# Kernel optimization log

Measured on AMD Instinct MI355X. Metric: run time of the kernel, lower is better.

The kernel has to match this reference:

```python
import jax, jax.numpy as jnp
import numpy as np

N_NODES = 200_000
N_EVENTS = 50_000
MEM = 128
RAW = 64
TD = 64
HEADS = 2
DH = MEM // HEADS
EDGE_DIM = RAW + TD
MSG_IN = 2 * MEM + RAW + TD


def _time_enc(x, w, b):
    # PyG TimeEncoder: cos(Linear(t)) with Linear(1, time_dim)
    return jnp.cos(x[..., None] * w + b)


def setup_inputs() -> dict:
    key = jax.random.key(0)
    ks = jax.random.split(key, 30)

    def w(i, shape, scale=None):
        s = scale if scale is not None else 1.0 / np.sqrt(shape[-1])
        return jax.random.normal(ks[i], shape, jnp.float32) * s

    src = jax.random.randint(ks[0], (N_EVENTS,), 0, N_NODES)
    dst = jax.random.randint(ks[1], (N_EVENTS,), 0, N_NODES)
    t = jnp.sort(jax.random.uniform(ks[2], (N_EVENTS,), jnp.float32, 0.0, 1e4))
    return dict(
        memory=w(3, (N_NODES, MEM), 1.0),
        last_update=jnp.zeros((N_NODES,), jnp.float32),
        t=t,
        msg=w(4, (N_EVENTS, RAW), 1.0),
        src=src, dst=dst,
        time_w=w(5, (TD,), 1.0), time_b=w(6, (TD,), 1.0),
        gru_Wih=w(7, (3 * MEM, MSG_IN)), gru_bih=w(8, (3 * MEM,), 0.02),
        gru_Whh=w(9, (3 * MEM, MEM)), gru_bhh=w(10, (3 * MEM,), 0.02),
        Wq=w(11, (MEM, MEM)), bq=w(12, (MEM,), 0.02),
        Wk=w(13, (MEM, MEM)), bk=w(14, (MEM,), 0.02),
        Wv=w(15, (MEM, MEM)), bv=w(16, (MEM,), 0.02),
        We=w(17, (MEM, EDGE_DIM)),
        Wskip=w(18, (MEM, MEM)), bskip=w(19, (MEM,), 0.02),
        Wls=w(20, (MEM, MEM)), bls=w(21, (MEM,), 0.02),
        Wld=w(22, (MEM, MEM)), bld=w(23, (MEM,), 0.02),
        Wlf=w(24, (1, MEM)), blf=w(25, (1,), 0.02),
    )


def reference(memory, last_update, t, msg, src, dst, time_w, time_b,
              gru_Wih, gru_bih, gru_Whh, gru_bhh,
              Wq, bq, Wk, bk, Wv, bv, We, Wskip, bskip,
              Wls, bls, Wld, bld, Wlf, blf):
    N, D = memory.shape
    E = src.shape[0]
    # --- 1. IdentityMessage: raw store for src side and dst side of each event ---
    dt_s = t - last_update[src]
    dt_d = t - last_update[dst]
    m_s = jnp.concatenate([memory[src], memory[dst], msg, _time_enc(dt_s, time_w, time_b)], -1)
    m_d = jnp.concatenate([memory[dst], memory[src], msg, _time_enc(dt_d, time_w, time_b)], -1)
    all_msg = jnp.concatenate([m_s, m_d], 0)        # [2E, MSG_IN]
    all_id = jnp.concatenate([src, dst], 0)         # [2E]
    all_t = jnp.concatenate([t, t], 0)              # [2E]
    # --- 2. LastAggregator: keep the latest message per target node ---
    pos = jnp.arange(2 * E, dtype=jnp.int32)
    last_pos = jnp.full((N,), -1, jnp.int32).at[all_id].max(pos)
    is_last = last_pos[all_id] == pos               # [2E], exactly one True per touched node
    # --- 3. GRUCell memory update (computed per message, scattered for the last one) ---
    h = memory[all_id]
    gi = all_msg @ gru_Wih.T + gru_bih
    gh = h @ gru_Whh.T + gru_bhh
    ir, iz, i_n = jnp.split(gi, 3, -1)
    hr, hz, h_n = jnp.split(gh, 3, -1)
    r = jax.nn.sigmoid(ir + hr)
    zg = jax.nn.sigmoid(iz + hz)
    n = jnp.tanh(i_n + r * h_n)
    h_new = (1.0 - zg) * n + zg * h
    memory_new = memory.at[all_id].add(jnp.where(is_last[:, None], h_new - h, 0.0))
    last_update_new = last_update.at[all_id].max(jnp.where(is_last, all_t, -jnp.inf))
    # --- 4. GraphAttentionEmbedding: TransformerConv(heads=2, edge_dim) in eval mode ---
    rel_t = last_update_new[src] - t
    edge_attr = jnp.concatenate([_time_enc(rel_t, time_w, time_b), msg], -1)  # [E, EDGE_DIM]
    e_proj = edge_attr @ We.T                                                  # [E, MEM]
    q = (memory_new @ Wq.T + bq).reshape(N, HEADS, DH)
    k = (memory_new[src] @ Wk.T + bk + e_proj).reshape(E, HEADS, DH)
    v = (memory_new[src] @ Wv.T + bv + e_proj).reshape(E, HEADS, DH)
    logit = jnp.einsum('ehd,ehd->eh', q[dst], k) / np.sqrt(DH).astype(np.float32)
    mx = jnp.full((N, HEADS), -jnp.inf, memory.dtype).at[dst].max(logit)
    a = jnp.exp(logit - mx[dst])
    denom = jax.ops.segment_sum(a, dst, num_segments=N)
    attn = a / denom[dst]                                                      # segment softmax over incoming edges
    out = jnp.zeros((N, HEADS, DH), memory.dtype).at[dst].add(attn[..., None] * v)
    z = out.reshape(N, D) + memory_new @ Wskip.T + bskip                       # root/skip connection
    # --- 5. LinkPredictor on event endpoints ---
    hlp = jax.nn.relu(z[src] @ Wls.T + bls + z[dst] @ Wld.T + bld)
    return hlp @ Wlf.T + blf                                                   # [E, 1]
```

## Files before the change

### kernel.cpp

```cpp
#include <hip/hip_runtime.h>
#include <math.h>

#define NN 200000
#define NE 50000
#define D 128
#define ZROW 256

#define WGRU_SZ  196608
#define WATTN_SZ 147456
#define WLNK2_SZ 65536

#define CVT0 102528
#define MEMB_V4 6400000
#define MSGB_V4 800000

__device__ __forceinline__ float frcp_(float x) { return __builtin_amdgcn_rcpf(x); }
__device__ __forceinline__ float fsig_(float x) { return frcp_(1.f + __expf(-x)); }
__device__ __forceinline__ float ftanh_(float x) {
    float xc = fminf(fmaxf(x, -15.f), 15.f);
    float t = __expf(2.f * xc);
    return (t - 1.f) * frcp_(t + 1.f);
}

__device__ __forceinline__ unsigned short f2bf(float f) {
    unsigned int u = __float_as_uint(f);
    u = (u + 0x7fffu + ((u >> 16) & 1u)) >> 16;
    return (unsigned short)u;
}
__device__ __forceinline__ float bf2f(unsigned short b) {
    return __uint_as_float(((unsigned int)b) << 16);
}

typedef short bf16x8 __attribute__((ext_vector_type(8)));
typedef float f32x4  __attribute__((ext_vector_type(4)));

__global__ void k_initprep(const float* __restrict__ Wih, const float* __restrict__ Whh,
                           const float* __restrict__ Wk, const float* __restrict__ Wv,
                           const float* __restrict__ Wq, const float* __restrict__ We,
                           const float* __restrict__ Wskip, const float* __restrict__ bskip,
                           const float* __restrict__ Wls, const float* __restrict__ Wld,
                           const float* __restrict__ bls, const float* __restrict__ bld,
                           const int* __restrict__ src, const int* __restrict__ dst,
                           const float* __restrict__ memory, const float* __restrict__ msg,
                           unsigned short* __restrict__ wgru,
                           unsigned short* __restrict__ wattn,
                           unsigned short* __restrict__ wlink2,
                           float* __restrict__ blink,
                           unsigned short* __restrict__ memb,
                           unsigned short* __restrict__ msgb,
                           int* __restrict__ last_pos, int* __restrict__ count) {
    int idx = blockIdx.x * 256 + threadIdx.x;
    if (idx == 0) *count = 0;
    if (idx < 2 * NE) {
        int id = (idx < NE) ? src[idx] : dst[idx - NE];
        atomicMax(&last_pos[id], idx + 1);
    }
    if (idx >= CVT0) {
        int j = idx - CVT0;
        if (j < MEMB_V4) {
            float4 v = ((const float4*)memory)[j];
            ushort4 b;
            b.x = f2bf(v.x); b.y = f2bf(v.y); b.z = f2bf(v.z); b.w = f2bf(v.w);
            ((ushort4*)memb)[j] = b;
        } else {
            j -= MEMB_V4;
            if (j < MSGB_V4) {
                float4 v = ((const float4*)msg)[j];
                ushort4 b;
                b.x = f2bf(v.x); b.y = f2bf(v.y); b.z = f2bf(v.z); b.w = f2bf(v.w);
                ((ushort4*)msgb)[j] = b;
            }
        }
        return;
    }
    float4 v;
    unsigned short* dstp;
    int ncopies, stride;
    if (idx < 49152) {
        int n = idx / 96;
        int c = (idx - n * 96) * 4;
        if (n < 384) {
            v = *(const float4*)&Wih[n * 384 + c];
            if (n < 256 && c < 128) {
                const float4 w2 = *(const float4*)&Whh[n * 128 + c];
                v.x += w2.x; v.y += w2.y; v.z += w2.z; v.w += w2.w;
            }
        } else {
            if (c >= 128) return;
            v = *(const float4*)&Whh[(n - 128) * 128 + c];
        }
        dstp = &wgru[n * 384 + c]; ncopies = 8; stride = WGRU_SZ;
    } else if (idx < 49152 + 36864) {
        int i2 = idx - 49152;
        int n = i2 / 96;
        int c = (i2 - n * 96) * 4;
        if (n < 256) {
            const float* Wm = (n < 128) ? Wk : Wv;
            int nn = n & 127;
            if (c < 128)       v = *(const float4*)&Wm[nn * 128 + c];
            else if (c < 256)  v = *(const float4*)&We[nn * 128 + (c - 128)];
            else return;
        } else {
            if (c < 256) return;
            v = *(const float4*)&Wq[(n - 256) * 128 + (c - 256)];
        }
        dstp = &wattn[n * 384 + c]; ncopies = 4; stride = WATTN_SZ;
    } else if (idx < 86016 + 8192) {
        int i4 = idx - 86016;
        int n = i4 >> 6;
        int c = (i4 & 63) * 4;
        int dc;
        if (c < 128) { v = *(const float4*)&Wls[n * 128 + c];        dc = c; }
        else         { v = *(const float4*)&Wld[n * 128 + (c - 128)]; dc = c + 128; }
        dstp = &wlink2[n * 512 + dc]; ncopies = 4; stride = WLNK2_SZ;
    } else if (idx < 94208 + 8192) {
        int i5 = idx - 94208;
        int n = i5 >> 6;
        int g = i5 & 63;
        const float* Wrow = (g < 32) ? &Wls[n * 128] : &Wld[n * 128];
        int c = (g & 31) * 4;
        float ax = 0.f, ay = 0.f, az = 0.f, aw = 0.f;
        for (int j = 0; j < 128; ++j) {
            float a = Wrow[j];
            const float4 ws = *(const float4*)&Wskip[j * 128 + c];
            ax += a * ws.x; ay += a * ws.y; az += a * ws.z; aw += a * ws.w;
        }
        ushort4 b4;
        b4.x = f2bf(ax); b4.y = f2bf(ay); b4.z = f2bf(az); b4.w = f2bf(aw);
        unsigned short* dp = &wlink2[n * 512 + ((g < 32) ? 128 : 384) + c];
        for (int r = 0; r < 4; ++r)
            *(ushort4*)(dp + (size_t)r * WLNK2_SZ) = b4;
        return;
    } else {
        int n = idx - 102400;
        float s = bls[n] + bld[n];
        for (int j = 0; j < 128; ++j)
            s += (Wls[n * 128 + j] + Wld[n * 128 + j]) * bskip[j];
        blink[n] = s;
        return;
    }
    ushort4 b;
    b.x = f2bf(v.x); b.y = f2bf(v.y); b.z = f2bf(v.z); b.w = f2bf(v.w);
    for (int r = 0; r < ncopies; ++r)
        *(ushort4*)(dstp + (size_t)r * stride) = b;
}

__global__ void k_compact(const int* __restrict__ src, const int* __restrict__ dst,
                          const int* __restrict__ last_pos,
                          const float* __restrict__ tp, const float* __restrict__ lup,
                          int* __restrict__ count, int* __restrict__ node2slot,
                          int* __restrict__ head,
                          int4* __restrict__ slot_aux,
                          float* __restrict__ lu_new) {
    int i = blockIdx.x * blockDim.x + threadIdx.x;
    if (i >= 2 * NE) return;
    int e  = (i < NE) ? i : i - NE;
    int id = (i < NE) ? src[e] : dst[e];
    if (last_pos[id] != i + 1) return;
    int s = atomicAdd(count, 1);
    node2slot[id] = s;
    head[s] = -1;
    int oth = (i < NE) ? dst[e] : src[e];
    float tt = tp[e];
    float lu = lup[id];
    lu_new[id] = fmaxf(lu, tt);
    int4 aux; aux.x = e; aux.y = oth; aux.z = __float_as_int(tt - lu); aux.w = id;
    slot_aux[s] = aux;
}

#define GMB 64
__global__ __launch_bounds__(512) void k_gru(
    const unsigned short* __restrict__ msgb,
    const float* __restrict__ twp, const float* __restrict__ tbp,
    const int4* __restrict__ slot_aux,
    const unsigned short* __restrict__ memb,
    const unsigned short* __restrict__ wgru_all,
    const float* __restrict__ bih, const float* __restrict__ bhh,
    const int* __restrict__ countp,
    unsigned short* __restrict__ zcat)
{
    __shared__ alignas(16) unsigned short Xs[64][392];
    int cnt = *countp;
    int base = blockIdx.x * GMB;
    if (base >= cnt) return;
    int tid = threadIdx.x;
    const unsigned short* __restrict__ wgru = wgru_all + (size_t)(blockIdx.x & 7) * WGRU_SZ;

    {
        int m = tid >> 3, li = tid & 7;
        int ii = base + m; if (ii >= cnt) ii = cnt - 1;
        const int4 aux = slot_aux[ii];
        int e = aux.x, oth = aux.y, id = aux.w;
        float dt = __int_as_float(aux.z);
        const uint4* idr  = (const uint4*)(memb + (size_t)id  * D);
        const uint4* othr = (const uint4*)(memb + (size_t)oth * D);
        uint4 A0 = idr[li],  A1 = idr[li + 8];
        uint4 B0 = othr[li], B1 = othr[li + 8];
        uint4 M0 = *(const uint4*)&msgb[e * 64 + li * 8];
        int c0 = li * 8;
        float cv[8];
        #pragma unroll
        for (int k = 0; k < 8; ++k)
            cv[k] = cosf(dt * twp[c0 + k] + tbp[c0 + k]);
        *(uint4*)&Xs[m][li * 8]        = A0;
        *(uint4*)&Xs[m][64 + li * 8]   = A1;
        *(uint4*)&Xs[m][128 + li * 8]  = B0;
        *(uint4*)&Xs[m][192 + li * 8]  = B1;
        *(uint4*)&Xs[m][256 + li * 8]  = M0;
        ushort4 t0, t1;
        t0.x = f2bf(cv[0]); t0.y = f2bf(cv[1]); t0.z = f2bf(cv[2]); t0.w = f2bf(cv[3]);
        t1.x = f2bf(cv[4]); t1.y = f2bf(cv[5]); t1.z = f2bf(cv[6]); t1.w = f2bf(cv[7]);
        *(ushort4*)&Xs[m][320 + c0]     = t0;
        *(ushort4*)&Xs[m][320 + c0 + 4] = t1;
    }
    __syncthreads();

    int lane = tid & 63, w = tid >> 6;
    int q = lane >> 4, l15 = lane & 15;
    int q8 = q * 8, w16 = w * 16;

    f32x4 acc[4][4];
    #pragma unroll
    for (int mt = 0; mt < 4; ++mt)
        #pragma unroll
        for (int g = 0; g < 4; ++g)
            acc[mt][g] = (f32x4)(0.0f);

#define GRU_STEP(NG)                                                                      \
    {                                                                                     \
        bf16x8 a[4];                                                                      \
        _Pragma("unroll")                                                                 \
        for (int mt = 0; mt < 4; ++mt) a[mt] = *(const bf16x8*)&Xs[mt * 16 + l15][k0 + q8]; \
        _Pragma("unroll")                                                                 \
        for (int g = 0; g < NG; ++g) {                                                    \
            const bf16x8 b = *(const bf16x8*)&wgru[(g * 128 + w16 + l15) * 384 + k0 + q8]; \
            _Pragma("unroll")                                                             \
            for (int mt = 0; mt < 4; ++mt)                                                \
                acc[mt][g] = __builtin_amdgcn_mfma_f32_16x16x32_bf16(a[mt], b, acc[mt][g], 0, 0, 0); \
        }                                                                                 \
    }

    #pragma unroll 2
    for (int ks = 0; ks < 4; ++ks) { int k0 = ks * 32; GRU_STEP(4) }
    #pragma unroll 2
    for (int ks = 4; ks < 12; ++ks) { int k0 = ks * 32; GRU_STEP(3) }
#undef GRU_STEP

    float nval[4][4];
    {
        int c = w16 + l15;
        float br  = bih[c]       + bhh[c];
        float bz  = bih[128 + c] + bhh[128 + c];
        float bin = bih[256 + c];
        float bhn = bhh[256 + c];
        #pragma unroll
        for (int mt = 0; mt < 4; ++mt) {
            #pragma unroll
            for (int reg = 0; reg < 4; ++reg) {
                int m = mt * 16 + q * 4 + reg;
                float r  = fsig_(acc[mt][0][reg] + br);
                float zg = fsig_(acc[mt][1][reg] + bz);
                float n  = ftanh_(acc[mt][2][reg] + bin + r * (acc[mt][3][reg] + bhn));
                float hv = bf2f(Xs[m][c]);
                nval[mt][reg] = (1.f - zg) * n + zg * hv;
            }
        }
    }

    __syncthreads();
    {
        int c = w16 + l15;
        #pragma unroll
        for (int mt = 0; mt < 4; ++mt)
            #pragma unroll
            for (int reg = 0; reg < 4; ++reg)
                Xs[mt * 16 + q * 4 + reg][c] = f2bf(nval[mt][reg]);
    }
    __syncthreads();

    {
        #pragma unroll
        for (int j = 0; j < 2; ++j) {
            int ch = tid + 512 * j;
            int m = ch >> 4, c8 = ch & 15;
            *(uint4*)&zcat[(size_t)(base + m) * ZROW + 128 + c8 * 8] =
                *(const uint4*)&Xs[m][c8 * 8];
        }
    }
}

#define AMB 32
__global__ __launch_bounds__(256) void k_attnA(
    const int* __restrict__ srcp, const int* __restrict__ dstp,
    const float* __restrict__ tp, const unsigned short* __restrict__ msgb,
    const float* __restrict__ twp, const float* __restrict__ tbp,
    const float* __restrict__ lu_new, const int* __restrict__ node2slot,
    const unsigned short* __restrict__ zcat,
    const unsigned short* __restrict__ wattn_all,
    const float* __restrict__ bq, const float* __restrict__ bk, const float* __restrict__ bv,
    unsigned short* __restrict__ vbuf, float* __restrict__ abuf,
    int* __restrict__ head, int* __restrict__ next)
{
    __shared__ alignas(16) unsigned short Xs[32][392];
    unsigned short (*kLb)[136] = (unsigned short(*)[136])(&Xs[0][0]);
    unsigned short (*qLb)[136] = (unsigned short(*)[136])(&Xs[0][0] + 4352);
    __shared__ float sa[AMB][2];
    __shared__ int sslot[AMB], sdslot[AMB];
    __shared__ float srel[AMB];
    int tid = threadIdx.x;
    int e0 = blockIdx.x * AMB;
    const unsigned short* __restrict__ wattn = wattn_all + (size_t)(blockIdx.x & 3) * WATTN_SZ;
    {
        int gid = blockIdx.x * 256 + tid;
        if (gid < NE) {
            int sl = node2slot[dstp[gid]];
            next[gid] = atomicExch(&head[sl], gid);
        }
    }
    if (tid < AMB) {
        int e = e0 + tid; if (e >= NE) e = NE - 1;
        int s = srcp[e], dd = dstp[e];
        sslot[tid]  = node2slot[s];
        sdslot[tid] = node2slot[dd];
        srel[tid] = lu_new[s] - tp[e];
    }
    __syncthreads();
    {
        int m = tid >> 3, li = tid & 7;
        int e = e0 + m; if (e >= NE) e = NE - 1;
        int ssl = sslot[m], dsl = sdslot[m];
        float rel = srel[m];
        uint4* xrow = (uint4*)&Xs[m][0];
        const uint4* srow = (const uint4*)&zcat[(size_t)ssl * ZROW + 128];
        const uint4* drow = (const uint4*)&zcat[(size_t)dsl * ZROW + 128];
        #pragma unroll
        for (int j = 0; j < 2; ++j) {
            xrow[li + 8 * j]      = srow[li + 8 * j];
            xrow[32 + li + 8 * j] = drow[li + 8 * j];
        }
        {
            int c0 = li * 8;
            ushort4 lo, hi;
            lo.x = f2bf(cosf(rel * twp[c0 + 0] + tbp[c0 + 0]));
            lo.y = f2bf(cosf(rel * twp[c0 + 1] + tbp[c0 + 1]));
            lo.z = f2bf(cosf(rel * twp[c0 + 2] + tbp[c0 + 2]));
            lo.w = f2bf(cosf(rel * twp[c0 + 3] + tbp[c0 + 3]));
            hi.x = f2bf(cosf(rel * twp[c0 + 4] + tbp[c0 + 4]));
            hi.y = f2bf(cosf(rel * twp[c0 + 5] + tbp[c0 + 5]));
            hi.z = f2bf(cosf(rel * twp[c0 + 6] + tbp[c0 + 6]));
            hi.w = f2bf(cosf(rel * twp[c0 + 7] + tbp[c0 + 7]));
            *(ushort4*)&Xs[m][128 + c0]     = lo;
            *(ushort4*)&Xs[m][128 + c0 + 4] = hi;
        }
        *(uint4*)&Xs[m][192 + li * 8] = *(const uint4*)&msgb[e * 64 + li * 8];
    }
    __syncthreads();

    int lane = tid & 63, w = tid >> 6;
    int q = lane >> 4, l15 = lane & 15;
    int q8 = q * 8;

    f32x4 acc[2][6];
    #pragma unroll
    for (int mt = 0; mt < 2; ++mt)
        #pragma unroll
        for (int jj = 0; jj < 6; ++jj) acc[mt][jj] = (f32x4)(0.0f);

    #pragma unroll 2
    for (int ks = 0; ks < 8; ++ks) {
        int k0 = ks * 32;
        const bf16x8 a0 = *(const bf16x8*)&Xs[l15][k0 + q8];
        const bf16x8 a1 = *(const bf16x8*)&Xs[16 + l15][k0 + q8];
        #pragma unroll
        for (int jj = 0; jj < 4; ++jj) {
            int nt = w + 4 * jj;
            const bf16x8 b = *(const bf16x8*)&wattn[(nt * 16 + l15) * 384 + k0 + q8];
            acc[0][jj] = __builtin_amdgcn_mfma_f32_16x16x32_bf16(a0, b, acc[0][jj], 0, 0, 0);
            acc[1][jj] = __builtin_amdgcn_mfma_f32_16x16x32_bf16(a1, b, acc[1][jj], 0, 0, 0);
        }
    }
    #pragma unroll 2
    for (int ks = 8; ks < 12; ++ks) {
        int k0 = ks * 32;
        const bf16x8 a0 = *(const bf16x8*)&Xs[l15][k0 + q8];
        const bf16x8 a1 = *(const bf16x8*)&Xs[16 + l15][k0 + q8];
        #pragma unroll
        for (int jj = 4; jj < 6; ++jj) {
            int nt = w + 4 * jj;
            const bf16x8 b = *(const bf16x8*)&wattn[(nt * 16 + l15) * 384 + k0 + q8];
            acc[0][jj] = __builtin_amdgcn_mfma_f32_16x16x32_bf16(a0, b, acc[0][jj], 0, 0, 0);
            acc[1][jj] = __builtin_amdgcn_mfma_f32_16x16x32_bf16(a1, b, acc[1][jj], 0, 0, 0);
        }
    }

    __syncthreads();

    float vreg[2][2][4];
    #pragma unroll
    for (int jj = 0; jj < 6; ++jj) {
        int nt = w + 4 * jj;
        int gate = nt >> 3;
        int ch = (nt & 7) * 16 + l15;
        float bias = (gate == 0) ? bk[ch] : (gate == 1) ? bv[ch] : bq[ch];
        #pragma unroll
        for (int mt = 0; mt < 2; ++mt)
            #pragma unroll
            for (int reg = 0; reg < 4; ++reg) {
                int m = mt * 16 + q * 4 + reg;
                float val = acc[mt][jj][reg] + bias;
                if (gate == 0)      kLb[m][ch] = f2bf(val);
                else if (gate == 2) qLb[m][ch] = f2bf(val);
                else                vreg[jj - 2][mt][reg] = val;
            }
    }
    __syncthreads();
    #pragma unroll
    for (int pr = 0; pr < 16; ++pr) {
        int p2 = pr * 4 + w;
        int m = p2 >> 1, h = p2 & 1;
        float prod = bf2f(qLb[m][h * 64 + lane]) * bf2f(kLb[m][h * 64 + lane]);
        #pragma unroll
        for (int off = 32; off; off >>= 1) prod += __shfl_down(prod, off);
        if (lane == 0) {
            float a = __expf(prod * 0.125f);
            sa[m][h] = a;
            if (e0 + m < NE) abuf[(e0 + m) * 2 + h] = a;
        }
    }
    __syncthreads();
    {
        unsigned short (*vL)[136] = qLb;
        #pragma unroll
        for (int jv = 0; jv < 2; ++jv) {
            int ch = w * 16 + jv * 64 + l15;
            int h = jv;
            #pragma unroll
            for (int mt = 0; mt < 2; ++mt)
                #pragma unroll
                for (int reg = 0; reg < 4; ++reg) {
                    int m = mt * 16 + q * 4 + reg;
                    vL[m][ch] = f2bf(sa[m][h] * vreg[jv][mt][reg]);
                }
        }
        __syncthreads();
        #pragma unroll
        for (int j = 0; j < 2; ++j) {
            int chunk = tid + 256 * j;
            int row = chunk >> 4, c8 = chunk & 15;
            if (e0 + row < NE)
                *(uint4*)&vbuf[(size_t)(e0 + row) * D + c8 * 8] = *(const uint4*)&vL[row][c8 * 8];
        }
    }
}

__global__ __launch_bounds__(256) void k_gather(
    const int* __restrict__ countp, const int* __restrict__ head,
    const int* __restrict__ next, const float* __restrict__ abuf,
    const unsigned short* __restrict__ vbuf, unsigned short* __restrict__ zcat)
{
    int cnt = *countp;
    int slot = blockIdx.x * 32 + (threadIdx.x >> 3);
    if (slot >= cnt) return;
    int li = threadIdx.x & 7;
    int c0 = li * 16;
    int h = li >> 2;
    float vsum[16];
    #pragma unroll
    for (int j = 0; j < 16; ++j) vsum[j] = 0.f;
    float asum = 0.f;
    for (int e = head[slot]; e != -1; e = next[e]) {
        asum += abuf[e * 2 + h];
        uint4 v0 = *(const uint4*)&vbuf[(size_t)e * D + c0];
        uint4 v1 = *(const uint4*)&vbuf[(size_t)e * D + c0 + 8];
        const unsigned short* pv0 = (const unsigned short*)&v0;
        const unsigned short* pv1 = (const unsigned short*)&v1;
        #pragma unroll
        for (int j = 0; j < 8; ++j) { vsum[j] += bf2f(pv0[j]); vsum[8 + j] += bf2f(pv1[j]); }
    }
    float rr = (asum > 0.f) ? frcp_(asum) : 0.f;
    unsigned short o[16];
    #pragma unroll
    for (int j = 0; j < 16; ++j) o[j] = f2bf(vsum[j] * rr);
    *(uint4*)&zcat[(size_t)slot * ZROW + c0]     = *(const uint4*)&o[0];
    *(uint4*)&zcat[(size_t)slot * ZROW + c0 + 8] = *(const uint4*)&o[8];
}

#define ALB 32
__global__ __launch_bounds__(256) void k_link(
    const int* __restrict__ srcp, const int* __restrict__ dstp,
    const int* __restrict__ node2slot,
    const unsigned short* __restrict__ zcat,
    const unsigned short* __restrict__ wlink2_all,
    const float* __restrict__ blink,
    const float* __restrict__ Wlf, const float* __restrict__ blf,
    float* __restrict__ outp)
{
    __shared__ alignas(16) unsigned short Xs[32][520];
    __shared__ int ssl[32], sdl[32];
    __shared__ float sred[32][4];
    int tid = threadIdx.x;
    int e0 = blockIdx.x * ALB;
    const unsigned short* __restrict__ wlink2 = wlink2_all + (size_t)(blockIdx.x & 3) * WLNK2_SZ;
    if (tid < ALB) {
        int e = e0 + tid; if (e >= NE) e = NE - 1;
        ssl[tid] = node2slot[srcp[e]];
        sdl[tid] = node2slot[dstp[e]];
    }
    __syncthreads();
    {
        int m = tid >> 3, li = tid & 7;
        uint4* xrow = (uint4*)&Xs[m][0];
        const uint4* srow = (const uint4*)&zcat[(size_t)ssl[m] * ZROW];
        const uint4* drow = (const uint4*)&zcat[(size_t)sdl[m] * ZROW];
        #pragma unroll
        for (int j = 0; j < 4; ++j) {
            xrow[li + 8 * j]      = srow[li + 8 * j];
            xrow[32 + li + 8 * j] = drow[li + 8 * j];
        }
    }
    __syncthreads();

    int lane = tid & 63, w = tid >> 6;
    int q = lane >> 4, l15 = lane & 15;
    int q8 = q * 8;

    f32x4 acc[2][2];
    #pragma unroll
    for (int mt = 0; mt < 2; ++mt)
        #pragma unroll
        for (int jj = 0; jj < 2; ++jj) acc[mt][jj] = (f32x4)(0.0f);

    #pragma unroll 2
    for (int ks = 0; ks < 16; ++ks) {
        int k0 = ks * 32;
        bf16x8 a[2];
        #pragma unroll
        for (int mt = 0; mt < 2; ++mt) a[mt] = *(const bf16x8*)&Xs[mt * 16 + l15][k0 + q8];
        #pragma unroll
        for (int jj = 0; jj < 2; ++jj) {
            int nt = w + 4 * jj;
            const bf16x8 b = *(const bf16x8*)&wlink2[(nt * 16 + l15) * 512 + k0 + q8];
            #pragma unroll
            for (int mt = 0; mt < 2; ++mt)
                acc[mt][jj] = __builtin_amdgcn_mfma_f32_16x16x32_bf16(a[mt], b, acc[mt][jj], 0, 0, 0);
        }
    }

    float p[2][4];
    #pragma unroll
    for (int mt = 0; mt < 2; ++mt)
        #pragma unroll
        for (int reg = 0; reg < 4; ++reg) p[mt][reg] = 0.f;
    #pragma unroll
    for (int jj = 0; jj < 2; ++jj) {
        int ch = (w + 4 * jj) * 16 + l15;
        float bias = blink[ch];
        float wl = Wlf[ch];
        #pragma unroll
        for (int mt = 0; mt < 2; ++mt)
            #pragma unroll
            for (int reg = 0; reg < 4; ++reg)
                p[mt][reg] += fmaxf(acc[mt][jj][reg] + bias, 0.f) * wl;
    }
    #pragma unroll
    for (int mask = 1; mask < 16; mask <<= 1) {
        #pragma unroll
        for (int mt = 0; mt < 2; ++mt)
            #pragma unroll
            for (int reg = 0; reg < 4; ++reg)
                p[mt][reg] += __shfl_xor(p[mt][reg], mask);
    }
    if (l15 == 0) {
        #pragma unroll
        for (int mt = 0; mt < 2; ++mt)
            #pragma unroll
            for (int reg = 0; reg < 4; ++reg)
                sred[mt * 16 + q * 4 + reg][w] = p[mt][reg];
    }
    __syncthreads();
    if (tid < ALB) {
        int e = e0 + tid;
        if (e < NE)
            outp[e] = sred[tid][0] + sred[tid][1] + sred[tid][2] + sred[tid][3] + blf[0];
    }
}

extern "C" void kernel_launch(void* const* d_in, const int* in_sizes, int n_in,
                              void* d_out, int out_size, void* d_ws, size_t ws_size,
                              hipStream_t stream)
{
    const float* memory      = (const float*)d_in[0];
    const float* last_update = (const float*)d_in[1];
    const float* t           = (const float*)d_in[2];
    const float* msg         = (const float*)d_in[3];
    const int*   src         = (const int*)d_in[4];
    const int*   dst         = (const int*)d_in[5];
    const float* time_w      = (const float*)d_in[6];
    const float* time_b      = (const float*)d_in[7];
    const float* gru_Wih     = (const float*)d_in[8];
    const float* gru_bih     = (const float*)d_in[9];
    const float* gru_Whh     = (const float*)d_in[10];
    const float* gru_bhh     = (const float*)d_in[11];
    const float* Wq          = (const float*)d_in[12];
    const float* bq          = (const float*)d_in[13];
    const float* Wk          = (const float*)d_in[14];
    const float* bk          = (const float*)d_in[15];
    const float* Wv          = (const float*)d_in[16];
    const float* bv          = (const float*)d_in[17];
    const float* We          = (const float*)d_in[18];
    const float* Wskip       = (const float*)d_in[19];
    const float* bskip       = (const float*)d_in[20];
    const float* Wls         = (const float*)d_in[21];
    const float* bls         = (const float*)d_in[22];
    const float* Wld         = (const float*)d_in[23];
    const float* bld         = (const float*)d_in[24];
    const float* Wlf         = (const float*)d_in[25];
    const float* blf         = (const float*)d_in[26];
    float* outp = (float*)d_out;

    char* ws = (char*)d_ws;
    int*   last_pos  = (int*)  (ws + 0);
    int*   node2slot = (int*)  (ws + 800000);
    float* lu_new    = (float*)(ws + 1600000);
    int*   count     = (int*)  (ws + 2400000);
    unsigned short* wlink2  = (unsigned short*)(ws + 2800016);
    float* blink   = (float*)(ws + 3324304);
    int4*  slot_aux = (int4*)(ws + 4000000);
    unsigned short* memb    = (unsigned short*)(ws + 6000000);
    unsigned short* msgb    = (unsigned short*)(ws + 57200000);
    unsigned short* wgru    = (unsigned short*)(ws + 79624592);
    unsigned short* wattn   = (unsigned short*)(ws + 82770320);
    unsigned short* zcat    = (unsigned short*)(ws + 84474256);
    unsigned short* vbuf    = (unsigned short*)(ws + 135690640);
    float* abuf = (float*)(ws + 148490640);
    int*   head = (int*)  (ws + 148890640);
    int*   next = (int*)  (ws + 149290768);

    k_initprep<<<(CVT0 + MEMB_V4 + MSGB_V4 + 255) / 256, 256, 0, stream>>>(
                 gru_Wih, gru_Whh, Wk, Wv, Wq, We, Wskip, bskip, Wls, Wld, bls, bld,
                 src, dst, memory, msg, wgru, wattn, wlink2, blink, memb, msgb,
                 last_pos, count);
    k_compact <<<(2 * NE + 255) / 256, 256, 0, stream>>>(src, dst, last_pos,
                 t, last_update, count, node2slot, head, slot_aux, lu_new);
    k_gru     <<<(2 * NE + GMB - 1) / GMB, 512, 0, stream>>>(msgb, time_w, time_b,
                 slot_aux, memb, wgru, gru_bih, gru_bhh, count, zcat);
    k_attnA   <<<(NE + AMB - 1) / AMB, 256, 0, stream>>>(src, dst, t, msgb, time_w, time_b,
                 lu_new, node2slot, zcat, wattn, bq, bk, bv, vbuf, abuf, head, next);
    k_gather  <<<(2 * NE + 31) / 32, 256, 0, stream>>>(count, head, next, abuf, vbuf, zcat);
    k_link    <<<(NE + ALB - 1) / ALB, 256, 0, stream>>>(src, dst, node2slot, zcat,
                 wlink2, blink, Wlf, blf, outp);
}
```

Before: 426.2 us.

## Convert only touched memory rows to bf16 and shrink GRU tile to 32 rows

The full conversion of the 200k-row memory table to bf16 is replaced by a new kernel that converts only the rows of nodes touched by events into a compact per-slot buffer. It also remaps each slot's partner node to its slot index so the GRU can read the compact buffer directly. The GRU kernel changes from 64-row, 512-thread blocks to 32-row, 256-thread blocks, with each wave now covering two 16-column subtiles. This removes roughly 100 MB of memory traffic, at the cost of an extra launch and a random-row gather from fp32 memory.

```diff
diff --git a/kernel.cpp b/kernel.cpp
--- a/kernel.cpp
+++ b/kernel.cpp
@@ -11,7 +11,6 @@
 #define WLNK2_SZ 65536
 
 #define CVT0 102528
-#define MEMB_V4 6400000
 #define MSGB_V4 800000
 
 __device__ __forceinline__ float frcp_(float x) { return __builtin_amdgcn_rcpf(x); }
@@ -41,12 +40,11 @@
                            const float* __restrict__ Wls, const float* __restrict__ Wld,
                            const float* __restrict__ bls, const float* __restrict__ bld,
                            const int* __restrict__ src, const int* __restrict__ dst,
-                           const float* __restrict__ memory, const float* __restrict__ msg,
+                           const float* __restrict__ msg,
                            unsigned short* __restrict__ wgru,
                            unsigned short* __restrict__ wattn,
                            unsigned short* __restrict__ wlink2,
                            float* __restrict__ blink,
-                           unsigned short* __restrict__ memb,
                            unsigned short* __restrict__ msgb,
                            int* __restrict__ last_pos, int* __restrict__ count) {
     int idx = blockIdx.x * 256 + threadIdx.x;
@@ -57,19 +55,11 @@
     }
     if (idx >= CVT0) {
         int j = idx - CVT0;
-        if (j < MEMB_V4) {
-            float4 v = ((const float4*)memory)[j];
+        if (j < MSGB_V4) {
+            float4 v = ((const float4*)msg)[j];
             ushort4 b;
             b.x = f2bf(v.x); b.y = f2bf(v.y); b.z = f2bf(v.z); b.w = f2bf(v.w);
-            ((ushort4*)memb)[j] = b;
-        } else {
-            j -= MEMB_V4;
-            if (j < MSGB_V4) {
-                float4 v = ((const float4*)msg)[j];
-                ushort4 b;
-                b.x = f2bf(v.x); b.y = f2bf(v.y); b.z = f2bf(v.z); b.w = f2bf(v.w);
-                ((ushort4*)msgb)[j] = b;
-            }
+            ((ushort4*)msgb)[j] = b;
         }
         return;
     }
@@ -168,18 +158,40 @@
     slot_aux[s] = aux;
 }
 
-#define GMB 64
-__global__ __launch_bounds__(512) void k_gru(
+__global__ __launch_bounds__(256) void k_memcvt(
+    const float* __restrict__ memory, const int* __restrict__ node2slot,
+    const int* __restrict__ countp,
+    int4* __restrict__ slot_aux, unsigned short* __restrict__ mco)
+{
+    int cnt = *countp;
+    int s = blockIdx.x * 32 + (threadIdx.x >> 3);
+    if (s >= cnt) return;
+    int li = threadIdx.x & 7;
+    int4 aux = slot_aux[s];
+    const float4* mrow = (const float4*)(memory + (size_t)aux.w * D);
+    ushort4* orow = (ushort4*)(mco + (size_t)s * D);
+    #pragma unroll
+    for (int j = 0; j < 4; ++j) {
+        float4 v = mrow[li + 8 * j];
+        ushort4 b;
+        b.x = f2bf(v.x); b.y = f2bf(v.y); b.z = f2bf(v.z); b.w = f2bf(v.w);
+        orow[li + 8 * j] = b;
+    }
+    if (li == 0) slot_aux[s].y = node2slot[aux.y];
+}
+
+#define GMB 32
+__global__ __launch_bounds__(256) void k_gru(
     const unsigned short* __restrict__ msgb,
     const float* __restrict__ twp, const float* __restrict__ tbp,
     const int4* __restrict__ slot_aux,
-    const unsigned short* __restrict__ memb,
+    const unsigned short* __restrict__ mco,
     const unsigned short* __restrict__ wgru_all,
     const float* __restrict__ bih, const float* __restrict__ bhh,
     const int* __restrict__ countp,
     unsigned short* __restrict__ zcat)
 {
-    __shared__ alignas(16) unsigned short Xs[64][392];
+    __shared__ alignas(16) unsigned short Xs[32][392];
     int cnt = *countp;
     int base = blockIdx.x * GMB;
     if (base >= cnt) return;
@@ -190,10 +202,10 @@
         int m = tid >> 3, li = tid & 7;
         int ii = base + m; if (ii >= cnt) ii = cnt - 1;
         const int4 aux = slot_aux[ii];
-        int e = aux.x, oth = aux.y, id = aux.w;
+        int e = aux.x, oslot = aux.y;
         float dt = __int_as_float(aux.z);
-        const uint4* idr  = (const uint4*)(memb + (size_t)id  * D);
-        const uint4* othr = (const uint4*)(memb + (size_t)oth * D);
+        const uint4* idr  = (const uint4*)(mco + (size_t)ii    * D);
+        const uint4* othr = (const uint4*)(mco + (size_t)oslot * D);
         uint4 A0 = idr[li],  A1 = idr[li + 8];
         uint4 B0 = othr[li], B1 = othr[li + 8];
         uint4 M0 = *(const uint4*)&msgb[e * 64 + li * 8];
@@ -217,26 +229,31 @@
 
     int lane = tid & 63, w = tid >> 6;
     int q = lane >> 4, l15 = lane & 15;
-    int q8 = q * 8, w16 = w * 16;
-
-    f32x4 acc[4][4];
-    #pragma unroll
-    for (int mt = 0; mt < 4; ++mt)
+    int q8 = q * 8, w32 = w * 32;
+
+    f32x4 acc[2][4][2];
+    #pragma unroll
+    for (int mt = 0; mt < 2; ++mt)
         #pragma unroll
         for (int g = 0; g < 4; ++g)
-            acc[mt][g] = (f32x4)(0.0f);
+            #pragma unroll
+            for (int ns = 0; ns < 2; ++ns)
+                acc[mt][g][ns] = (f32x4)(0.0f);
 
 #define GRU_STEP(NG)                                                                      \
     {                                                                                     \
-        bf16x8 a[4];                                                                      \
+        bf16x8 a[2];                                                                      \
         _Pragma("unroll")                                                                 \
-        for (int mt = 0; mt < 4; ++mt) a[mt] = *(const bf16x8*)&Xs[mt * 16 + l15][k0 + q8]; \
+        for (int mt = 0; mt < 2; ++mt) a[mt] = *(const bf16x8*)&Xs[mt * 16 + l15][k0 + q8]; \
         _Pragma("unroll")                                                                 \
         for (int g = 0; g < NG; ++g) {                                                    \
-            const bf16x8 b = *(const bf16x8*)&wgru[(g * 128 + w16 + l15) * 384 + k0 + q8]; \
             _Pragma("unroll")                                                             \
-            for (int mt = 0; mt < 4; ++mt)                                                \
-                acc[mt][g] = __builtin_amdgcn_mfma_f32_16x16x32_bf16(a[mt], b, acc[mt][g], 0, 0, 0); \
+            for (int ns = 0; ns < 2; ++ns) {                                              \
+                const bf16x8 b = *(const bf16x8*)&wgru[(g * 128 + w32 + ns * 16 + l15) * 384 + k0 + q8]; \
+                _Pragma("unroll")                                                         \
+                for (int mt = 0; mt < 2; ++mt)                                            \
+                    acc[mt][g][ns] = __builtin_amdgcn_mfma_f32_16x16x32_bf16(a[mt], b, acc[mt][g][ns], 0, 0, 0); \
+            }                                                                             \
         }                                                                                 \
     }
 
@@ -246,42 +263,44 @@
     for (int ks = 4; ks < 12; ++ks) { int k0 = ks * 32; GRU_STEP(3) }
 #undef GRU_STEP
 
-    float nval[4][4];
-    {
-        int c = w16 + l15;
+    float nval[2][2][4];
+    #pragma unroll
+    for (int ns = 0; ns < 2; ++ns) {
+        int c = w32 + ns * 16 + l15;
         float br  = bih[c]       + bhh[c];
         float bz  = bih[128 + c] + bhh[128 + c];
         float bin = bih[256 + c];
         float bhn = bhh[256 + c];
         #pragma unroll
-        for (int mt = 0; mt < 4; ++mt) {
+        for (int mt = 0; mt < 2; ++mt) {
             #pragma unroll
             for (int reg = 0; reg < 4; ++reg) {
                 int m = mt * 16 + q * 4 + reg;
-                float r  = fsig_(acc[mt][0][reg] + br);
-                float zg = fsig_(acc[mt][1][reg] + bz);
-                float n  = ftanh_(acc[mt][2][reg] + bin + r * (acc[mt][3][reg] + bhn));
+                float r  = fsig_(acc[mt][0][ns][reg] + br);
+                float zg = fsig_(acc[mt][1][ns][reg] + bz);
+                float n  = ftanh_(acc[mt][2][ns][reg] + bin + r * (acc[mt][3][ns][reg] + bhn));
                 float hv = bf2f(Xs[m][c]);
-                nval[mt][reg] = (1.f - zg) * n + zg * hv;
+                nval[mt][ns][reg] = (1.f - zg) * n + zg * hv;
             }
         }
     }
 
     __syncthreads();
+    #pragma unroll
+    for (int ns = 0; ns < 2; ++ns) {
+        int c = w32 + ns * 16 + l15;
+        #pragma unroll
+        for (int mt = 0; mt < 2; ++mt)
+            #pragma unroll
+            for (int reg = 0; reg < 4; ++reg)
+                Xs[mt * 16 + q * 4 + reg][c] = f2bf(nval[mt][ns][reg]);
+    }
+    __syncthreads();
+
     {
-        int c = w16 + l15;
-        #pragma unroll
-        for (int mt = 0; mt < 4; ++mt)
-            #pragma unroll
-            for (int reg = 0; reg < 4; ++reg)
-                Xs[mt * 16 + q * 4 + reg][c] = f2bf(nval[mt][reg]);
-    }
-    __syncthreads();
-
-    {
         #pragma unroll
         for (int j = 0; j < 2; ++j) {
-            int ch = tid + 512 * j;
+            int ch = tid + 256 * j;
             int m = ch >> 4, c8 = ch & 15;
             *(uint4*)&zcat[(size_t)(base + m) * ZROW + 128 + c8 * 8] =
                 *(const uint4*)&Xs[m][c8 * 8];
@@ -626,7 +645,7 @@
     unsigned short* wlink2  = (unsigned short*)(ws + 2800016);
     float* blink   = (float*)(ws + 3324304);
     int4*  slot_aux = (int4*)(ws + 4000000);
-    unsigned short* memb    = (unsigned short*)(ws + 6000000);
+    unsigned short* mco     = (unsigned short*)(ws + 6000000);
     unsigned short* msgb    = (unsigned short*)(ws + 57200000);
     unsigned short* wgru    = (unsigned short*)(ws + 79624592);
     unsigned short* wattn   = (unsigned short*)(ws + 82770320);
@@ -636,14 +655,15 @@
     int*   head = (int*)  (ws + 148890640);
     int*   next = (int*)  (ws + 149290768);
 
-    k_initprep<<<(CVT0 + MEMB_V4 + MSGB_V4 + 255) / 256, 256, 0, stream>>>(
+    k_initprep<<<(CVT0 + MSGB_V4 + 255) / 256, 256, 0, stream>>>(
                  gru_Wih, gru_Whh, Wk, Wv, Wq, We, Wskip, bskip, Wls, Wld, bls, bld,
-                 src, dst, memory, msg, wgru, wattn, wlink2, blink, memb, msgb,
-                 last_pos, count);
+                 src, dst, msg, wgru, wattn, wlink2, blink, msgb, last_pos, count);
     k_compact <<<(2 * NE + 255) / 256, 256, 0, stream>>>(src, dst, last_pos,
                  t, last_update, count, node2slot, head, slot_aux, lu_new);
-    k_gru     <<<(2 * NE + GMB - 1) / GMB, 512, 0, stream>>>(msgb, time_w, time_b,
-                 slot_aux, memb, wgru, gru_bih, gru_bhh, count, zcat);
+    k_memcvt  <<<(2 * NE + 31) / 32, 256, 0, stream>>>(memory, node2slot, count,
+                 slot_aux, mco);
+    k_gru     <<<(2 * NE + GMB - 1) / GMB, 256, 0, stream>>>(msgb, time_w, time_b,
+                 slot_aux, mco, wgru, gru_bih, gru_bhh, count, zcat);
     k_attnA   <<<(NE + AMB - 1) / AMB, 256, 0, stream>>>(src, dst, t, msgb, time_w, time_b,
                  lu_new, node2slot, zcat, wattn, bq, bk, bv, vbuf, abuf, head, next);
     k_gather  <<<(2 * NE + 31) / 32, 256, 0, stream>>>(count, head, next, abuf, vbuf, zcat);
```

Result: slower. 465.9 us (+9.3%).

## Convert only touched memory rows to bf16 per slot; widen attention tile to 64 events

Applied to the files above, without the earlier changes.

Drops the full-table fp32-to-bf16 conversion of the node memory. A new kernel converts only the rows of nodes that appear in events, stores them compactly by slot, and rewrites each slot's partner id to its slot index so the GRU kernel reads compact rows. Separately, the attention kernel now processes 64 events per 512-thread block with a reorganised MFMA tiling, reusing each weight fragment across four row tiles. This removes large bandwidth-bound prep traffic at the cost of one extra launch and a serial dependency on compaction.

```diff
diff --git a/kernel.cpp b/kernel.cpp
--- a/kernel.cpp
+++ b/kernel.cpp
@@ -11,7 +11,6 @@
 #define WLNK2_SZ 65536
 
 #define CVT0 102528
-#define MEMB_V4 6400000
 #define MSGB_V4 800000
 
 __device__ __forceinline__ float frcp_(float x) { return __builtin_amdgcn_rcpf(x); }
@@ -41,12 +40,11 @@
                            const float* __restrict__ Wls, const float* __restrict__ Wld,
                            const float* __restrict__ bls, const float* __restrict__ bld,
                            const int* __restrict__ src, const int* __restrict__ dst,
-                           const float* __restrict__ memory, const float* __restrict__ msg,
+                           const float* __restrict__ msg,
                            unsigned short* __restrict__ wgru,
                            unsigned short* __restrict__ wattn,
                            unsigned short* __restrict__ wlink2,
                            float* __restrict__ blink,
-                           unsigned short* __restrict__ memb,
                            unsigned short* __restrict__ msgb,
                            int* __restrict__ last_pos, int* __restrict__ count) {
     int idx = blockIdx.x * 256 + threadIdx.x;
@@ -57,19 +55,11 @@
     }
     if (idx >= CVT0) {
         int j = idx - CVT0;
-        if (j < MEMB_V4) {
-            float4 v = ((const float4*)memory)[j];
+        if (j < MSGB_V4) {
+            float4 v = ((const float4*)msg)[j];
             ushort4 b;
             b.x = f2bf(v.x); b.y = f2bf(v.y); b.z = f2bf(v.z); b.w = f2bf(v.w);
-            ((ushort4*)memb)[j] = b;
-        } else {
-            j -= MEMB_V4;
-            if (j < MSGB_V4) {
-                float4 v = ((const float4*)msg)[j];
-                ushort4 b;
-                b.x = f2bf(v.x); b.y = f2bf(v.y); b.z = f2bf(v.z); b.w = f2bf(v.w);
-                ((ushort4*)msgb)[j] = b;
-            }
+            ((ushort4*)msgb)[j] = b;
         }
         return;
     }
@@ -168,12 +158,34 @@
     slot_aux[s] = aux;
 }
 
+__global__ __launch_bounds__(256) void k_memcvt(
+    const float* __restrict__ memory, const int* __restrict__ node2slot,
+    const int* __restrict__ countp,
+    int4* __restrict__ slot_aux, unsigned short* __restrict__ mco)
+{
+    int cnt = *countp;
+    int s = blockIdx.x * 32 + (threadIdx.x >> 3);
+    if (s >= cnt) return;
+    int li = threadIdx.x & 7;
+    int4 aux = slot_aux[s];
+    const float4* mrow = (const float4*)(memory + (size_t)aux.w * D);
+    ushort4* orow = (ushort4*)(mco + (size_t)s * D);
+    #pragma unroll
+    for (int j = 0; j < 4; ++j) {
+        float4 v = mrow[li + 8 * j];
+        ushort4 b;
+        b.x = f2bf(v.x); b.y = f2bf(v.y); b.z = f2bf(v.z); b.w = f2bf(v.w);
+        orow[li + 8 * j] = b;
+    }
+    if (li == 0) slot_aux[s].y = node2slot[aux.y];
+}
+
 #define GMB 64
 __global__ __launch_bounds__(512) void k_gru(
     const unsigned short* __restrict__ msgb,
     const float* __restrict__ twp, const float* __restrict__ tbp,
     const int4* __restrict__ slot_aux,
-    const unsigned short* __restrict__ memb,
+    const unsigned short* __restrict__ mco,
     const unsigned short* __restrict__ wgru_all,
     const float* __restrict__ bih, const float* __restrict__ bhh,
     const int* __restrict__ countp,
@@ -190,10 +202,10 @@
         int m = tid >> 3, li = tid & 7;
         int ii = base + m; if (ii >= cnt) ii = cnt - 1;
         const int4 aux = slot_aux[ii];
-        int e = aux.x, oth = aux.y, id = aux.w;
+        int e = aux.x, oslot = aux.y;
         float dt = __int_as_float(aux.z);
-        const uint4* idr  = (const uint4*)(memb + (size_t)id  * D);
-        const uint4* othr = (const uint4*)(memb + (size_t)oth * D);
+        const uint4* idr  = (const uint4*)(mco + (size_t)ii    * D);
+        const uint4* othr = (const uint4*)(mco + (size_t)oslot * D);
         uint4 A0 = idr[li],  A1 = idr[li + 8];
         uint4 B0 = othr[li], B1 = othr[li + 8];
         uint4 M0 = *(const uint4*)&msgb[e * 64 + li * 8];
@@ -289,8 +301,8 @@
     }
 }
 
-#define AMB 32
-__global__ __launch_bounds__(256) void k_attnA(
+#define AMB 64
+__global__ __launch_bounds__(512) void k_attnA(
     const int* __restrict__ srcp, const int* __restrict__ dstp,
     const float* __restrict__ tp, const unsigned short* __restrict__ msgb,
     const float* __restrict__ twp, const float* __restrict__ tbp,
@@ -301,9 +313,9 @@
     unsigned short* __restrict__ vbuf, float* __restrict__ abuf,
     int* __restrict__ head, int* __restrict__ next)
 {
-    __shared__ alignas(16) unsigned short Xs[32][392];
+    __shared__ alignas(16) unsigned short Xs[64][392];
     unsigned short (*kLb)[136] = (unsigned short(*)[136])(&Xs[0][0]);
-    unsigned short (*qLb)[136] = (unsigned short(*)[136])(&Xs[0][0] + 4352);
+    unsigned short (*qLb)[136] = (unsigned short(*)[136])(&Xs[0][0] + 8704);
     __shared__ float sa[AMB][2];
     __shared__ int sslot[AMB], sdslot[AMB];
     __shared__ float srel[AMB];
@@ -311,7 +323,7 @@
     int e0 = blockIdx.x * AMB;
     const unsigned short* __restrict__ wattn = wattn_all + (size_t)(blockIdx.x & 3) * WATTN_SZ;
     {
-        int gid = blockIdx.x * 256 + tid;
+        int gid = blockIdx.x * 512 + tid;
         if (gid < NE) {
             int sl = node2slot[dstp[gid]];
             next[gid] = atomicExch(&head[sl], gid);
@@ -360,63 +372,64 @@
     int q = lane >> 4, l15 = lane & 15;
     int q8 = q * 8;
 
-    f32x4 acc[2][6];
-    #pragma unroll
-    for (int mt = 0; mt < 2; ++mt)
-        #pragma unroll
-        for (int jj = 0; jj < 6; ++jj) acc[mt][jj] = (f32x4)(0.0f);
+    f32x4 acc[4][3];
+    #pragma unroll
+    for (int mt = 0; mt < 4; ++mt)
+        #pragma unroll
+        for (int jj = 0; jj < 3; ++jj) acc[mt][jj] = (f32x4)(0.0f);
 
     #pragma unroll 2
     for (int ks = 0; ks < 8; ++ks) {
         int k0 = ks * 32;
-        const bf16x8 a0 = *(const bf16x8*)&Xs[l15][k0 + q8];
-        const bf16x8 a1 = *(const bf16x8*)&Xs[16 + l15][k0 + q8];
-        #pragma unroll
-        for (int jj = 0; jj < 4; ++jj) {
-            int nt = w + 4 * jj;
+        bf16x8 a[4];
+        #pragma unroll
+        for (int mt = 0; mt < 4; ++mt) a[mt] = *(const bf16x8*)&Xs[mt * 16 + l15][k0 + q8];
+        #pragma unroll
+        for (int jj = 0; jj < 2; ++jj) {
+            int nt = w + 8 * jj;
             const bf16x8 b = *(const bf16x8*)&wattn[(nt * 16 + l15) * 384 + k0 + q8];
-            acc[0][jj] = __builtin_amdgcn_mfma_f32_16x16x32_bf16(a0, b, acc[0][jj], 0, 0, 0);
-            acc[1][jj] = __builtin_amdgcn_mfma_f32_16x16x32_bf16(a1, b, acc[1][jj], 0, 0, 0);
+            #pragma unroll
+            for (int mt = 0; mt < 4; ++mt)
+                acc[mt][jj] = __builtin_amdgcn_mfma_f32_16x16x32_bf16(a[mt], b, acc[mt][jj], 0, 0, 0);
         }
     }
     #pragma unroll 2
     for (int ks = 8; ks < 12; ++ks) {
         int k0 = ks * 32;
-        const bf16x8 a0 = *(const bf16x8*)&Xs[l15][k0 + q8];
-        const bf16x8 a1 = *(const bf16x8*)&Xs[16 + l15][k0 + q8];
-        #pragma unroll
-        for (int jj = 4; jj < 6; ++jj) {
-            int nt = w + 4 * jj;
-            const bf16x8 b = *(const bf16x8*)&wattn[(nt * 16 + l15) * 384 + k0 + q8];
-            acc[0][jj] = __builtin_amdgcn_mfma_f32_16x16x32_bf16(a0, b, acc[0][jj], 0, 0, 0);
-            acc[1][jj] = __builtin_amdgcn_mfma_f32_16x16x32_bf16(a1, b, acc[1][jj], 0, 0, 0);
-        }
-    }
-
-    __syncthreads();
-
-    float vreg[2][2][4];
-    #pragma unroll
-    for (int jj = 0; jj < 6; ++jj) {
-        int nt = w + 4 * jj;
-        int gate = nt >> 3;
-        int ch = (nt & 7) * 16 + l15;
-        float bias = (gate == 0) ? bk[ch] : (gate == 1) ? bv[ch] : bq[ch];
-        #pragma unroll
-        for (int mt = 0; mt < 2; ++mt)
-            #pragma unroll
-            for (int reg = 0; reg < 4; ++reg) {
-                int m = mt * 16 + q * 4 + reg;
-                float val = acc[mt][jj][reg] + bias;
-                if (gate == 0)      kLb[m][ch] = f2bf(val);
-                else if (gate == 2) qLb[m][ch] = f2bf(val);
-                else                vreg[jj - 2][mt][reg] = val;
-            }
+        bf16x8 a[4];
+        #pragma unroll
+        for (int mt = 0; mt < 4; ++mt) a[mt] = *(const bf16x8*)&Xs[mt * 16 + l15][k0 + q8];
+        int nt = 16 + w;
+        const bf16x8 b = *(const bf16x8*)&wattn[(nt * 16 + l15) * 384 + k0 + q8];
+        #pragma unroll
+        for (int mt = 0; mt < 4; ++mt)
+            acc[mt][2] = __builtin_amdgcn_mfma_f32_16x16x32_bf16(a[mt], b, acc[mt][2], 0, 0, 0);
+    }
+
+    __syncthreads();
+
+    float vreg[4][4];
+    {
+        int ch = w * 16 + l15;
+        #pragma unroll
+        for (int jj = 0; jj < 3; ++jj) {
+            float bias = (jj == 0) ? bk[ch] : (jj == 1) ? bv[ch] : bq[ch];
+            #pragma unroll
+            for (int mt = 0; mt < 4; ++mt)
+                #pragma unroll
+                for (int reg = 0; reg < 4; ++reg) {
+                    int m = mt * 16 + q * 4 + reg;
+                    float val = acc[mt][jj][reg] + bias;
+                    if (jj == 0)      kLb[m][ch] = f2bf(val);
+                    else if (jj == 2) qLb[m][ch] = f2bf(val);
+                    else              vreg[mt][reg] = val;
+                }
+        }
     }
     __syncthreads();
     #pragma unroll
     for (int pr = 0; pr < 16; ++pr) {
-        int p2 = pr * 4 + w;
+        int p2 = pr * 8 + w;
         int m = p2 >> 1, h = p2 & 1;
         float prod = bf2f(qLb[m][h * 64 + lane]) * bf2f(kLb[m][h * 64 + lane]);
         #pragma unroll
@@ -430,22 +443,19 @@
     __syncthreads();
     {
         unsigned short (*vL)[136] = qLb;
-        #pragma unroll
-        for (int jv = 0; jv < 2; ++jv) {
-            int ch = w * 16 + jv * 64 + l15;
-            int h = jv;
-            #pragma unroll
-            for (int mt = 0; mt < 2; ++mt)
-                #pragma unroll
-                for (int reg = 0; reg < 4; ++reg) {
-                    int m = mt * 16 + q * 4 + reg;
-                    vL[m][ch] = f2bf(sa[m][h] * vreg[jv][mt][reg]);
-                }
-        }
+        int ch = w * 16 + l15;
+        int h = w >> 2;
+        #pragma unroll
+        for (int mt = 0; mt < 4; ++mt)
+            #pragma unroll
+            for (int reg = 0; reg < 4; ++reg) {
+                int m = mt * 16 + q * 4 + reg;
+                vL[m][ch] = f2bf(sa[m][h] * vreg[mt][reg]);
+            }
         __syncthreads();
         #pragma unroll
         for (int j = 0; j < 2; ++j) {
-            int chunk = tid + 256 * j;
+            int chunk = tid + 512 * j;
             int row = chunk >> 4, c8 = chunk & 15;
             if (e0 + row < NE)
                 *(uint4*)&vbuf[(size_t)(e0 + row) * D + c8 * 8] = *(const uint4*)&vL[row][c8 * 8];
@@ -626,7 +636,7 @@
     unsigned short* wlink2  = (unsigned short*)(ws + 2800016);
     float* blink   = (float*)(ws + 3324304);
     int4*  slot_aux = (int4*)(ws + 4000000);
-    unsigned short* memb    = (unsigned short*)(ws + 6000000);
+    unsigned short* mco     = (unsigned short*)(ws + 6000000);
     unsigned short* msgb    = (unsigned short*)(ws + 57200000);
     unsigned short* wgru    = (unsigned short*)(ws + 79624592);
     unsigned short* wattn   = (unsigned short*)(ws + 82770320);
@@ -636,15 +646,16 @@
     int*   head = (int*)  (ws + 148890640);
     int*   next = (int*)  (ws + 149290768);
 
-    k_initprep<<<(CVT0 + MEMB_V4 + MSGB_V4 + 255) / 256, 256, 0, stream>>>(
+    k_initprep<<<(CVT0 + MSGB_V4 + 255) / 256, 256, 0, stream>>>(
                  gru_Wih, gru_Whh, Wk, Wv, Wq, We, Wskip, bskip, Wls, Wld, bls, bld,
-                 src, dst, memory, msg, wgru, wattn, wlink2, blink, memb, msgb,
-                 last_pos, count);
+                 src, dst, msg, wgru, wattn, wlink2, blink, msgb, last_pos, count);
     k_compact <<<(2 * NE + 255) / 256, 256, 0, stream>>>(src, dst, last_pos,
                  t, last_update, count, node2slot, head, slot_aux, lu_new);
+    k_memcvt  <<<(2 * NE + 31) / 32, 256, 0, stream>>>(memory, node2slot, count,
+                 slot_aux, mco);
     k_gru     <<<(2 * NE + GMB - 1) / GMB, 512, 0, stream>>>(msgb, time_w, time_b,
-                 slot_aux, memb, wgru, gru_bih, gru_bhh, count, zcat);
-    k_attnA   <<<(NE + AMB - 1) / AMB, 256, 0, stream>>>(src, dst, t, msgb, time_w, time_b,
+                 slot_aux, mco, wgru, gru_bih, gru_bhh, count, zcat);
+    k_attnA   <<<(NE + AMB - 1) / AMB, 512, 0, stream>>>(src, dst, t, msgb, time_w, time_b,
                  lu_new, node2slot, zcat, wattn, bq, bk, bv, vbuf, abuf, head, next);
     k_gather  <<<(2 * NE + 31) / 32, 256, 0, stream>>>(count, head, next, abuf, vbuf, zcat);
     k_link    <<<(NE + ALB - 1) / ALB, 256, 0, stream>>>(src, dst, node2slot, zcat,
```

Result: faster. 403.2 us (-5.4%).
